# Performance work log

Measured on AMD Instinct MI355X. Metric: run time of the kernel, lower is better.

The kernel has to match this reference:

```python
import jax, jax.numpy as jnp
import numpy as np
from jax import lax

B, N, C = 4, 16384, 384
HEADS, HD = 8, 48
ALPHA = 4.0
KS = 5
HH = WW = 128


def setup_inputs() -> dict:
    key = jax.random.key(0)
    ks = jax.random.split(key, 9)
    s = 0.02
    return {
        "x": jax.random.normal(ks[0], (B, N, C), jnp.float32),
        "W_qg": jax.random.normal(ks[1], (C, 2 * C), jnp.float32) * s,
        "W_kv": jax.random.normal(ks[2], (C, 2 * C), jnp.float32) * s,
        "W_proj": jax.random.normal(ks[3], (C, C), jnp.float32) * s,
        "b_proj": jnp.zeros((C,), jnp.float32),
        "pos_enc": jax.random.normal(ks[4], (1, N, C), jnp.float32) * 0.02,
        "power_p": jax.random.normal(ks[5], (1, HEADS, 1, HD), jnp.float32) * 0.5,
        "scale_p": jax.random.normal(ks[6], (1, 1, C), jnp.float32) * 0.5,
        "dwc_w": jax.random.normal(ks[7], (HD, 1, KS, KS), jnp.float32) * s,
        "dwc_b": jnp.zeros((HD,), jnp.float32),
        "H": HH,
        "W": WW,
    }


def _relu_pow(x, p):
    # relu(x) ** p with safe gradients at x <= 0
    r = jax.nn.relu(x)
    base = jnp.where(r > 0, r, 1.0)
    return jnp.where(r > 0, base ** p, 0.0)


def reference(x, W_qg, W_kv, W_proj, b_proj, pos_enc, power_p, scale_p, dwc_w, dwc_b, H, W):
    Bx, Nx, Cx = x.shape
    h = power_p.shape[1]
    hd = power_p.shape[-1]

    qg = x @ W_qg                      # [B,N,2C]
    q, g = qg[..., :Cx], qg[..., Cx:]
    kv = x @ W_kv                      # [B,N,2C] (sr_ratio == 1)
    k, v = kv[..., :Cx], kv[..., Cx:]
    n = Nx
    k = k + pos_enc

    scale = jax.nn.softplus(scale_p)            # [1,1,C]
    power = 1.0 + ALPHA * jax.nn.sigmoid(power_p)  # [1,h,1,hd]
    q = q / scale
    k = k / scale

    # [B,h,N,hd]
    q = q.reshape(Bx, Nx, h, hd).transpose(0, 2, 1, 3)
    k = k.reshape(Bx, n, h, hd).transpose(0, 2, 1, 3)
    v = v.reshape(Bx, n, h, hd).transpose(0, 2, 1, 3)

    q_pos = _relu_pow(q, power)
    q_neg = _relu_pow(-q, power)
    k_pos = _relu_pow(k, power)
    k_neg = _relu_pow(-k, power)

    q_sim = jnp.concatenate([q_pos, q_neg], axis=-1)   # [B,h,N,2hd]
    q_opp = jnp.concatenate([q_neg, q_pos], axis=-1)
    kk = jnp.concatenate([k_pos, k_neg], axis=-1)      # [B,h,n,2hd]
    v1, v2 = v[..., : hd // 2], v[..., hd // 2:]

    k_mean = kk.mean(axis=2, keepdims=True)            # [B,h,1,2hd]
    inv_n = 1.0 / n

    z_sim = 1.0 / (jnp.sum(q_sim * k_mean, axis=-1, keepdims=True) + 1e-6)
    kv1 = jnp.einsum('bhnd,bhne->bhde', kk, v1) * inv_n  # [B,h,2hd,hd/2]
    x_sim = jnp.einsum('bhnd,bhde->bhne', q_sim, kv1) * z_sim

    z_opp = 1.0 / (jnp.sum(q_opp * k_mean, axis=-1, keepdims=True) + 1e-6)
    kv2 = jnp.einsum('bhnd,bhne->bhde', kk, v2) * inv_n
    x_opp = jnp.einsum('bhnd,bhde->bhne', q_opp, kv2) * z_opp

    out = jnp.concatenate([x_sim, x_opp], axis=-1)     # [B,h,N,hd]
    out = out.transpose(0, 2, 1, 3).reshape(Bx, Nx, Cx)

    # depthwise conv gate on v
    v4 = v.reshape(Bx * h, H, W, hd).transpose(0, 3, 1, 2)  # [B*h, hd, H, W]
    vc = lax.conv_general_dilated(
        v4, dwc_w, window_strides=(1, 1), padding='SAME',
        feature_group_count=hd,
        dimension_numbers=('NCHW', 'OIHW', 'NCHW'))
    vc = vc + dwc_b[None, :, None, None]
    v_out = vc.reshape(Bx, Cx, Nx).transpose(0, 2, 1)  # [B,N,C]

    out = (out + v_out) * g
    out = out @ W_proj + b_proj
    return out
```

## Files before the change

### kernel.cpp

```cpp
#include <hip/hip_runtime.h>
#include <math.h>


#define NB 4
#define NTOK 16384
#define CDIM 384
#define NHEAD 8
#define HDIM 48
#define IMGH 128
#define IMGW 128

typedef unsigned short u16;
typedef unsigned int u32;
typedef __attribute__((ext_vector_type(8))) short bf16x8;
typedef __attribute__((ext_vector_type(4))) float f32x4;

__device__ __forceinline__ float bf2f(u16 u) {
  return __uint_as_float(((unsigned)u) << 16);
}
__device__ __forceinline__ u16 f2bf(float f) {
  unsigned u = __float_as_uint(f);
  u += 0x7FFF + ((u >> 16) & 1);
  return (u16)(u >> 16);
}
__device__ __forceinline__ float pow_mag(float r, float p) {
  if (r < 1e-20f) return 0.0f;
  return exp2f(fminf(p * log2f(r), 80.0f));
}
__device__ __forceinline__ float ldx1(const void* p, size_t i, bool f32) {
  return f32 ? ((const float*)p)[i] : bf2f(((const u16*)p)[i]);
}
__device__ __forceinline__ void gload16(u16* lds, const u16* g) {
  __builtin_amdgcn_global_load_lds(
      (const __attribute__((address_space(1))) u32*)g,
      (__attribute__((address_space(3))) u32*)lds, 16, 0, 0);
}

__global__ __launch_bounds__(256) void k0_detect(const void* __restrict__ x,
                                                 int* __restrict__ flag) {
  __shared__ int s[256];
  const u16* p = (const u16*)x;
  const int t = threadIdx.x;
  int good = 0;
#pragma unroll
  for (int i = 0; i < 16; ++i) {
    const u16 w = p[t * 16 + i];
    const int e = (w >> 7) & 0xFF;
    good += (e >= 0x60 && e <= 0x85) ? 1 : 0;
  }
  s[t] = good;
  __syncthreads();
  for (int o = 128; o > 0; o >>= 1) {
    if (t < o) s[t] += s[t + o];
    __syncthreads();
  }
  if (t == 0) *flag = (s[0] >= (4096 * 4) / 5) ? 0 : 1;
}

__global__ __launch_bounds__(256) void kx_convert(const void* __restrict__ x,
                                                  const int* __restrict__ flag,
                                                  u16* __restrict__ xbf) {
  if (*flag == 0) return;
  const size_t S = (size_t)NB * NTOK * CDIM;
  const size_t tid = (size_t)blockIdx.x * 256 + threadIdx.x;
  const size_t stride = (size_t)gridDim.x * 256;
  const float4* xf = (const float4*)x;
  for (size_t i = tid; i < S / 8; i += stride) {
    const float4 a = xf[i * 2 + 0];
    const float4 b = xf[i * 2 + 1];
    *(ushort4*)(xbf + i * 8 + 0) = make_ushort4(f2bf(a.x), f2bf(a.y), f2bf(a.z), f2bf(a.w));
    *(ushort4*)(xbf + i * 8 + 4) = make_ushort4(f2bf(b.x), f2bf(b.y), f2bf(b.z), f2bf(b.w));
  }
}

__global__ __launch_bounds__(256) void kprep(
    const void* __restrict__ Wqg, const void* __restrict__ Wkv,
    const void* __restrict__ Wp, const int* __restrict__ flag,
    u16* __restrict__ W2T, u16* __restrict__ WpT)
{
  const bool f32 = (*flag != 0);
  const int idx = blockIdx.x * 256 + threadIdx.x;
  if (idx < 1536 * 384) {
    const int n = idx / 384, k = idx - n * 384;
    const float v = (n < 768) ? ldx1(Wqg, (size_t)k * 768 + n, f32)
                              : ldx1(Wkv, (size_t)k * 768 + (n - 768), f32);
    W2T[idx] = f2bf(v);
  } else {
    const int j = idx - 1536 * 384;
    if (j < 384 * 384) {
      const int n = j / 384, k = j - n * 384;
      WpT[j] = f2bf(ldx1(Wp, (size_t)k * 384 + n, f32));
    }
  }
}

__global__ __launch_bounds__(512) void k1_mfma(
    const void* __restrict__ x, const u16* __restrict__ xbf,
    const u16* __restrict__ W2T,
    const void* __restrict__ pos_enc, const void* __restrict__ scale_p,
    const int* __restrict__ flag, const int conv_ok,
    u16* __restrict__ qsT, u16* __restrict__ gT, u16* __restrict__ ksT, u16* __restrict__ vT)
{
  const bool f32 = (*flag != 0);
  const bool fast = (!f32) || (conv_ok != 0);
  const u16* Asrc = f32 ? xbf : (const u16*)x;
  __shared__ __align__(16) u16 smem[17408];
  u16* Asm = smem;
  u16* Bsm = smem + 8192;
  const int t = threadIdx.x;
  const int bid = blockIdx.x;
  const int rm = (bid & 7) * 768 + (bid >> 3);
  const int m_idx = rm / 12;
  const int n_idx = rm - m_idx * 12;
  const int n0 = n_idx * 128;
  const int m0 = m_idx * 128;
  const int wave = t >> 6, lane = t & 63;
  const int wr = wave >> 2, wc = wave & 3;
  const int lm = lane & 15, lq = lane >> 4;

  f32x4 acc[4][2] = {};

  auto STAGE = [&](int k0) {
#pragma unroll
    for (int i = 0; i < 2; ++i) {
      const int chunk = i * 512 + t;
      const int row = chunk >> 3, c8 = chunk & 7;
      const int sc8 = c8 ^ (row & 7);
      u16* lpA = &Asm[(i * 512 + wave * 64) * 8];
      u16* lpB = &Bsm[(i * 512 + wave * 64) * 8];
      gload16(lpA, Asrc + (size_t)(m0 + row) * CDIM + k0 + sc8 * 8);
      gload16(lpB, W2T + (size_t)(n0 + row) * CDIM + k0 + sc8 * 8);
    }
  };
  auto COMPUTE = [&]() {
#pragma unroll
    for (int kh = 0; kh < 2; ++kh) {
      bf16x8 af[4], bfr[2];
#pragma unroll
      for (int r = 0; r < 4; ++r) {
        const int row = wr * 64 + r * 16 + lm;
        af[r] = *(const bf16x8*)&Asm[row * 64 + (((kh * 4 + lq) ^ (row & 7)) * 8)];
      }
#pragma unroll
      for (int cb = 0; cb < 2; ++cb) {
        const int row = wc * 32 + cb * 16 + lm;
        bfr[cb] = *(const bf16x8*)&Bsm[row * 64 + (((kh * 4 + lq) ^ (row & 7)) * 8)];
      }
#pragma unroll
      for (int r = 0; r < 4; ++r)
#pragma unroll
        for (int cb = 0; cb < 2; ++cb)
          acc[r][cb] = __builtin_amdgcn_mfma_f32_16x16x32_bf16(af[r], bfr[cb], acc[r][cb], 0, 0, 0);
    }
  };

  if (fast) {
    for (int ks = 0; ks < 6; ++ks) {
      STAGE(ks * 64);
      __syncthreads();
      COMPUTE();
      __syncthreads();
    }
  } else {
    for (int k0 = 0; k0 < CDIM; k0 += 64) {
#pragma unroll
      for (int i = 0; i < 2; ++i) {
        const int chunk = t + i * 512;
        const int row = chunk >> 3, c8 = chunk & 7;
        const int ldsoff = row * 64 + ((c8 ^ (row & 7)) * 8);
        const float* xp = (const float*)x + (size_t)(m0 + row) * CDIM + k0 + c8 * 8;
        const float4 v0 = *(const float4*)xp;
        const float4 v1 = *(const float4*)(xp + 4);
        *(ushort4*)&Asm[ldsoff]     = make_ushort4(f2bf(v0.x), f2bf(v0.y), f2bf(v0.z), f2bf(v0.w));
        *(ushort4*)&Asm[ldsoff + 4] = make_ushort4(f2bf(v1.x), f2bf(v1.y), f2bf(v1.z), f2bf(v1.w));
        *(uint4*)&Bsm[ldsoff] = *(const uint4*)(W2T + (size_t)(n0 + row) * CDIM + k0 + c8 * 8);
      }
      __syncthreads();
      COMPUTE();
      __syncthreads();
    }
  }

  u16* et = smem;
  const int b = m0 >> 14;
  const int TOK0 = m0 & (NTOK - 1);
  const int region = n0 / CDIM;
#pragma unroll
  for (int cb = 0; cb < 2; ++cb) {
    const int cl = wc * 32 + cb * 16 + lm;
    const int c = (n0 - region * CDIM) + cl;
    float inv = 1.0f;
    if (region == 0 || region == 2) inv = 1.0f / log1pf(expf(ldx1(scale_p, c, f32)));
#pragma unroll
    for (int r = 0; r < 4; ++r) {
      const int tl = wr * 64 + r * 16 + lq * 4;
      const f32x4 v = acc[r][cb];
      ushort4 w;
      if (region == 2) {
        const int tok = TOK0 + tl;
        const float p0 = ldx1(pos_enc, (size_t)(tok + 0) * CDIM + c, f32);
        const float p1 = ldx1(pos_enc, (size_t)(tok + 1) * CDIM + c, f32);
        const float p2 = ldx1(pos_enc, (size_t)(tok + 2) * CDIM + c, f32);
        const float p3 = ldx1(pos_enc, (size_t)(tok + 3) * CDIM + c, f32);
        w = make_ushort4(f2bf((v[0] + p0) * inv), f2bf((v[1] + p1) * inv),
                         f2bf((v[2] + p2) * inv), f2bf((v[3] + p3) * inv));
      } else if (region == 0) {
        w = make_ushort4(f2bf(v[0] * inv), f2bf(v[1] * inv), f2bf(v[2] * inv), f2bf(v[3] * inv));
      } else {
        w = make_ushort4(f2bf(v[0]), f2bf(v[1]), f2bf(v[2]), f2bf(v[3]));
      }
      *(ushort4*)&et[cl * 136 + tl] = w;
    }
  }
  __syncthreads();
  u16* dst = (region == 0) ? qsT : (region == 1) ? gT : (region == 2) ? ksT : vT;
  const int cbase = b * CDIM + (n0 - region * CDIM);
#pragma unroll
  for (int i = 0; i < 4; ++i) {
    const int idx = i * 512 + t;
    const int row = idx >> 4, seg = idx & 15;
    const uint4 val = *(const uint4*)&et[row * 136 + seg * 8];
    *(uint4*)(dst + ((size_t)(cbase + row)) * NTOK + TOK0 + seg * 8) = val;
  }
}

__global__ __launch_bounds__(256) void k2_stats(
    const u16* __restrict__ ksT, const u16* __restrict__ vT,
    const void* __restrict__ power_p, const int* __restrict__ flag,
    float* __restrict__ km, float* __restrict__ kvm)
{
  const bool f32 = (*flag != 0);
  __shared__ __align__(16) u16 kkL[96][72];
  __shared__ __align__(16) u16 vL[48][72];
  __shared__ float pw[48];
  const int bh = blockIdx.x;
  const int b = bh >> 3, h = bh & 7;
  const int t = threadIdx.x;
  if (t < 48) pw[t] = 1.0f + 4.0f / (1.0f + expf(-ldx1(power_p, h * HDIM + t, f32)));
  __syncthreads();
  const int wave = t >> 6, lane = t & 63;
  const int lm = lane & 15, lq = lane >> 4;
  f32x4 acc[2][3] = {};
  float ksum = 0.0f;
  const u16* ksbase = ksT + ((size_t)(b * CDIM + h * HDIM)) * NTOK;
  const u16* vbase  = vT  + ((size_t)(b * CDIM + h * HDIM)) * NTOK;
  const int n0base = blockIdx.y * 1024;
  for (int tile = 0; tile < 16; ++tile) {
    const int n0 = n0base + tile * 64;
    for (int i = t; i < 48 * 16; i += 256) {
      const int c = i >> 4, qd = (i & 15) * 4;
      ushort4 kq = *(const ushort4*)(ksbase + (size_t)c * NTOK + n0 + qd);
      ushort4 vq = *(const ushort4*)(vbase  + (size_t)c * NTOK + n0 + qd);
      const float p = pw[c];
      float kf[4] = {bf2f(kq.x), bf2f(kq.y), bf2f(kq.z), bf2f(kq.w)};
      ushort4 pos, neg;
#pragma unroll
      for (int jj = 0; jj < 4; ++jj) {
        const float f = pow_mag(fabsf(kf[jj]), p);
        ((u16*)&pos)[jj] = f2bf((kf[jj] > 0.f) ? f : 0.f);
        ((u16*)&neg)[jj] = f2bf((kf[jj] < 0.f) ? f : 0.f);
      }
      *(ushort4*)&kkL[c][qd]      = pos;
      *(ushort4*)&kkL[c + 48][qd] = neg;
      *(ushort4*)&vL[c][qd]       = vq;
    }
    __syncthreads();
    if (wave < 3) {
      const int mbase = wave * 32;
#pragma unroll
      for (int kh = 0; kh < 2; ++kh) {
        bf16x8 af[2], bfr[3];
#pragma unroll
        for (int mi = 0; mi < 2; ++mi)
          af[mi] = *(const bf16x8*)&kkL[mbase + mi * 16 + lm][kh * 32 + lq * 8];
#pragma unroll
        for (int nj = 0; nj < 3; ++nj)
          bfr[nj] = *(const bf16x8*)&vL[nj * 16 + lm][kh * 32 + lq * 8];
#pragma unroll
        for (int mi = 0; mi < 2; ++mi)
#pragma unroll
          for (int nj = 0; nj < 3; ++nj)
            acc[mi][nj] = __builtin_amdgcn_mfma_f32_16x16x32_bf16(af[mi], bfr[nj], acc[mi][nj], 0, 0, 0);
      }
    }
    if (t < 96) {
#pragma unroll
      for (int nn = 0; nn < 64; nn += 4) {
        const ushort4 kq4 = *(const ushort4*)&kkL[t][nn];
        ksum += (bf2f(kq4.x) + bf2f(kq4.y)) + (bf2f(kq4.z) + bf2f(kq4.w));
      }
    }
    __syncthreads();
  }
  const float inv_n = 1.0f / (float)NTOK;
  if (wave < 3) {
    const int mbase = wave * 32;
#pragma unroll
    for (int mi = 0; mi < 2; ++mi)
#pragma unroll
      for (int nj = 0; nj < 3; ++nj) {
        const f32x4 v = acc[mi][nj];
#pragma unroll
        for (int reg = 0; reg < 4; ++reg) {
          const int d = mbase + mi * 16 + lq * 4 + reg;
          const int e = nj * 16 + lm;
          atomicAdd(&kvm[(size_t)bh * 96 * 48 + d * 48 + e], v[reg] * inv_n);
        }
      }
  }
  if (t < 96) atomicAdd(&km[bh * 96 + t], ksum * inv_n);
}

__global__ __launch_bounds__(256) void k3_attn(
    const u16* __restrict__ qsT, u16* __restrict__ attnT,
    const float* __restrict__ km_g, const float* __restrict__ kvm_g,
    const void* __restrict__ power_p, const int* __restrict__ flag)
{
  const bool f32 = (*flag != 0);
  __shared__ __align__(16) float kvmL[96][48];
  __shared__ float kmL[96];
  __shared__ float pw[48];
  const int bh = blockIdx.y;
  const int b = bh >> 3, h = bh & 7;
  const int t = threadIdx.x;
  for (int i = t; i < 96 * 48; i += 256) kvmL[i / 48][i % 48] = kvm_g[(size_t)bh * 96 * 48 + i];
  if (t < 96) kmL[t] = km_g[bh * 96 + t];
  if (t < 48) pw[t] = 1.0f + 4.0f / (1.0f + expf(-ldx1(power_p, h * HDIM + t, f32)));
  __syncthreads();
  const int n = blockIdx.x * 512 + t;
  const size_t chan0 = ((size_t)(b * CDIM + h * HDIM)) * NTOK + n;
  const u16* qbase = qsT + chan0;
  u16* obase = attnT + chan0;
  float4 accs[2][6] = {}, acco[2][6] = {};
  float zs[2] = {}, zo[2] = {};
  for (int d = 0; d < 48; ++d) {
    const float p = pw[d];
    float qp[2], qn[2];
#pragma unroll
    for (int i = 0; i < 2; ++i) {
      const float qv = bf2f(qbase[(size_t)d * NTOK + i * 256]);
      const float f = pow_mag(fabsf(qv), p);
      qp[i] = (qv > 0.f) ? f : 0.f;
      qn[i] = (qv < 0.f) ? f : 0.f;
      zs[i] = fmaf(qp[i], kmL[d], zs[i]); zs[i] = fmaf(qn[i], kmL[d + 48], zs[i]);
      zo[i] = fmaf(qn[i], kmL[d], zo[i]); zo[i] = fmaf(qp[i], kmL[d + 48], zo[i]);
    }
#pragma unroll
    for (int e4 = 0; e4 < 6; ++e4) {
      const float4 kvA = *(const float4*)&kvmL[d][e4 * 4];
      const float4 kvB = *(const float4*)&kvmL[d + 48][e4 * 4];
      const float4 kvC = *(const float4*)&kvmL[d][24 + e4 * 4];
      const float4 kvD = *(const float4*)&kvmL[d + 48][24 + e4 * 4];
#pragma unroll
      for (int i = 0; i < 2; ++i) {
        accs[i][e4].x = fmaf(qp[i], kvA.x, fmaf(qn[i], kvB.x, accs[i][e4].x));
        accs[i][e4].y = fmaf(qp[i], kvA.y, fmaf(qn[i], kvB.y, accs[i][e4].y));
        accs[i][e4].z = fmaf(qp[i], kvA.z, fmaf(qn[i], kvB.z, accs[i][e4].z));
        accs[i][e4].w = fmaf(qp[i], kvA.w, fmaf(qn[i], kvB.w, accs[i][e4].w));
        acco[i][e4].x = fmaf(qn[i], kvC.x, fmaf(qp[i], kvD.x, acco[i][e4].x));
        acco[i][e4].y = fmaf(qn[i], kvC.y, fmaf(qp[i], kvD.y, acco[i][e4].y));
        acco[i][e4].z = fmaf(qn[i], kvC.z, fmaf(qp[i], kvD.z, acco[i][e4].z));
        acco[i][e4].w = fmaf(qn[i], kvC.w, fmaf(qp[i], kvD.w, acco[i][e4].w));
      }
    }
  }
#pragma unroll
  for (int i = 0; i < 2; ++i) {
    const float zsi = 1.0f / (zs[i] + 1e-6f);
    const float zoi = 1.0f / (zo[i] + 1e-6f);
#pragma unroll
    for (int e4 = 0; e4 < 6; ++e4) {
      const float4 s = accs[i][e4], o = acco[i][e4];
      obase[(size_t)(e4 * 4 + 0) * NTOK + i * 256]    = f2bf(s.x * zsi);
      obase[(size_t)(e4 * 4 + 1) * NTOK + i * 256]    = f2bf(s.y * zsi);
      obase[(size_t)(e4 * 4 + 2) * NTOK + i * 256]    = f2bf(s.z * zsi);
      obase[(size_t)(e4 * 4 + 3) * NTOK + i * 256]    = f2bf(s.w * zsi);
      obase[(size_t)(24 + e4 * 4 + 0) * NTOK + i * 256] = f2bf(o.x * zoi);
      obase[(size_t)(24 + e4 * 4 + 1) * NTOK + i * 256] = f2bf(o.y * zoi);
      obase[(size_t)(24 + e4 * 4 + 2) * NTOK + i * 256] = f2bf(o.z * zoi);
      obase[(size_t)(24 + e4 * 4 + 3) * NTOK + i * 256] = f2bf(o.w * zoi);
    }
  }
}

__global__ __launch_bounds__(256) void k4_conv_combine(
    const u16* __restrict__ vT, const u16* __restrict__ gT,
    const void* __restrict__ dwc_w, const void* __restrict__ dwc_b,
    const int* __restrict__ flag,
    u16* __restrict__ attnT)
{
  const bool f32 = (*flag != 0);
  __shared__ float tile[20][136];
  const int bc = blockIdx.y;
  const int y0 = blockIdx.x * 16;
  const int t = threadIdx.x;
  const int d = bc % 48;
  float w[25];
#pragma unroll
  for (int i = 0; i < 25; ++i) w[i] = ldx1(dwc_w, d * 25 + i, f32);
  const float bias = ldx1(dwc_b, d, f32);
  const u16* vimg = vT + (size_t)bc * NTOK;
  for (int i = t; i < 20 * 34; i += 256) {
    const int r = i / 34, cq = (i - r * 34) * 4;
    const int gy = y0 + r - 2;
    float4 v4 = make_float4(0.f, 0.f, 0.f, 0.f);
    if (gy >= 0 && gy < IMGH) {
      const int gx0 = cq - 4;
      if (gx0 >= 0 && gx0 + 3 < IMGW) {
        const ushort4 u = *(const ushort4*)(vimg + gy * IMGW + gx0);
        v4 = make_float4(bf2f(u.x), bf2f(u.y), bf2f(u.z), bf2f(u.w));
      } else {
#pragma unroll
        for (int jj = 0; jj < 4; ++jj) {
          const int gx = gx0 + jj;
          ((float*)&v4)[jj] = (gx >= 0 && gx < IMGW) ? bf2f(vimg[gy * IMGW + gx]) : 0.f;
        }
      }
    }
    *(float4*)&tile[r][cq] = v4;
  }
  __syncthreads();
  u16* abase = attnT + (size_t)bc * NTOK;
  const u16* gbase = gT + (size_t)bc * NTOK;
#pragma unroll
  for (int pass = 0; pass < 2; ++pass) {
    const int yy = pass * 8 + (t >> 5);
    const int x0 = (t & 31) * 4;
    float a0 = bias, a1 = bias, a2 = bias, a3 = bias;
#pragma unroll
    for (int dy = 0; dy < 5; ++dy) {
      const float* row = &tile[yy + dy][0];
      const float4 A = *(const float4*)&row[x0];
      const float4 B = *(const float4*)&row[x0 + 4];
      const float4 C = *(const float4*)&row[x0 + 8];
      const float c0 = A.z, c1 = A.w, c2 = B.x, c3 = B.y,
                  c4 = B.z, c5 = B.w, c6 = C.x, c7 = C.y;
      const float w0 = w[dy * 5 + 0], w1 = w[dy * 5 + 1], w2 = w[dy * 5 + 2],
                  w3 = w[dy * 5 + 3], w4 = w[dy * 5 + 4];
      a0 = fmaf(w0, c0, fmaf(w1, c1, fmaf(w2, c2, fmaf(w3, c3, fmaf(w4, c4, a0)))));
      a1 = fmaf(w0, c1, fmaf(w1, c2, fmaf(w2, c3, fmaf(w3, c4, fmaf(w4, c5, a1)))));
      a2 = fmaf(w0, c2, fmaf(w1, c3, fmaf(w2, c4, fmaf(w3, c5, fmaf(w4, c6, a2)))));
      a3 = fmaf(w0, c3, fmaf(w1, c4, fmaf(w2, c5, fmaf(w3, c6, fmaf(w4, c7, a3)))));
    }
    const int gidx = (y0 + yy) * IMGW + x0;
    const ushort4 at = *(const ushort4*)(abase + gidx);
    const ushort4 gg = *(const ushort4*)(gbase + gidx);
    *(ushort4*)(abase + gidx) = make_ushort4(
        f2bf((bf2f(at.x) + a0) * bf2f(gg.x)),
        f2bf((bf2f(at.y) + a1) * bf2f(gg.y)),
        f2bf((bf2f(at.z) + a2) * bf2f(gg.z)),
        f2bf((bf2f(at.w) + a3) * bf2f(gg.w)));
  }
}

__global__ __launch_bounds__(256) void k4b_transpose(
    const u16* __restrict__ src,
    u16* __restrict__ dst)
{
  __shared__ u16 tile[64][68];
  const int b  = blockIdx.z;
  const int c0 = blockIdx.y * 64;
  const int n0 = blockIdx.x * 64;
  const int t = threadIdx.x;
  const int tr = t >> 4, tq = t & 15;
#pragma unroll
  for (int i = 0; i < 4; ++i) {
    const int r = tr + i * 16;
    *(ushort4*)&tile[r][tq * 4] =
        *(const ushort4*)(src + ((size_t)(b * CDIM + c0 + r)) * NTOK + n0 + tq * 4);
  }
  __syncthreads();
#pragma unroll
  for (int i = 0; i < 4; ++i) {
    const int n = tr + i * 16;
    const ushort4 vv = make_ushort4(tile[tq * 4 + 0][n], tile[tq * 4 + 1][n],
                                    tile[tq * 4 + 2][n], tile[tq * 4 + 3][n]);
    *(ushort4*)(dst + ((size_t)(b * NTOK + n0 + n)) * CDIM + c0 + tq * 4) = vv;
  }
}

__global__ __launch_bounds__(512) void k5_mfma(
    const u16* __restrict__ A,
    const u16* __restrict__ WpT,
    const void* __restrict__ bp, const int* __restrict__ flag,
    void* __restrict__ out)
{
  const bool f32 = (*flag != 0);
  __shared__ __align__(16) u16 smem[17408];
  u16* Asm = smem;
  u16* Bsm = smem + 8192;
  const int t = threadIdx.x;
  const int bid = blockIdx.x;
  const int rm = (bid & 7) * 192 + (bid >> 3);
  const int m_idx = rm / 3;
  const int n_idx = rm - m_idx * 3;
  const int n0 = n_idx * 128;
  const int m0 = m_idx * 128;
  const int wave = t >> 6, lane = t & 63;
  const int wr = wave >> 2, wc = wave & 3;
  const int lm = lane & 15, lq = lane >> 4;

  f32x4 acc[4][2] = {};

  auto STAGE = [&](int k0) {
#pragma unroll
    for (int i = 0; i < 2; ++i) {
      const int chunk = i * 512 + t;
      const int row = chunk >> 3, c8 = chunk & 7;
      const int sc8 = c8 ^ (row & 7);
      u16* lpA = &Asm[(i * 512 + wave * 64) * 8];
      u16* lpB = &Bsm[(i * 512 + wave * 64) * 8];
      gload16(lpA, A + (size_t)(m0 + row) * CDIM + k0 + sc8 * 8);
      gload16(lpB, WpT + (size_t)(n0 + row) * CDIM + k0 + sc8 * 8);
    }
  };
  auto COMPUTE = [&]() {
#pragma unroll
    for (int kh = 0; kh < 2; ++kh) {
      bf16x8 af[4], bfr[2];
#pragma unroll
      for (int r = 0; r < 4; ++r) {
        const int row = wr * 64 + r * 16 + lm;
        af[r] = *(const bf16x8*)&Asm[row * 64 + (((kh * 4 + lq) ^ (row & 7)) * 8)];
      }
#pragma unroll
      for (int cb = 0; cb < 2; ++cb) {
        const int row = wc * 32 + cb * 16 + lm;
        bfr[cb] = *(const bf16x8*)&Bsm[row * 64 + (((kh * 4 + lq) ^ (row & 7)) * 8)];
      }
#pragma unroll
      for (int r = 0; r < 4; ++r)
#pragma unroll
        for (int cb = 0; cb < 2; ++cb)
          acc[r][cb] = __builtin_amdgcn_mfma_f32_16x16x32_bf16(af[r], bfr[cb], acc[r][cb], 0, 0, 0);
    }
  };

  for (int ks = 0; ks < 6; ++ks) {
    STAGE(ks * 64);
    __syncthreads();
    COMPUTE();
    __syncthreads();
  }

  if (f32) {
    float* ef = (float*)smem;
    float bb[2];
#pragma unroll
    for (int cb = 0; cb < 2; ++cb) bb[cb] = ((const float*)bp)[n0 + wc * 32 + cb * 16 + lm];
    for (int h = 0; h < 2; ++h) {
      __syncthreads();
      if (wr == h) {
#pragma unroll
        for (int cb = 0; cb < 2; ++cb) {
          const int cl = wc * 32 + cb * 16 + lm;
#pragma unroll
          for (int r = 0; r < 4; ++r) {
            const int tl = r * 16 + lq * 4;
            const f32x4 v = acc[r][cb];
#pragma unroll
            for (int reg = 0; reg < 4; ++reg)
              ef[(tl + reg) * 132 + cl] = v[reg] + bb[cb];
          }
        }
      }
      __syncthreads();
      float* ob = (float*)out + (size_t)(m0 + h * 64) * CDIM + n0;
#pragma unroll
      for (int i = 0; i < 4; ++i) {
        const int idx = i * 512 + t;
        const int row = idx >> 5, seg = idx & 31;
        const float4 val = *(const float4*)&ef[row * 132 + seg * 4];
        *(float4*)(ob + (size_t)row * CDIM + seg * 4) = val;
      }
    }
  } else {
#pragma unroll
    for (int cb = 0; cb < 2; ++cb) {
      const int cg = n0 + wc * 32 + cb * 16 + lm;
      const float bbs = bf2f(((const u16*)bp)[cg]);
#pragma unroll
      for (int r = 0; r < 4; ++r) {
        const int rowtok = m0 + wr * 64 + r * 16 + lq * 4;
        const f32x4 v = acc[r][cb];
#pragma unroll
        for (int reg = 0; reg < 4; ++reg) {
          const size_t o = (size_t)(rowtok + reg) * CDIM + cg;
          ((u16*)out)[o] = f2bf(v[reg] + bbs);
        }
      }
    }
  }
}

extern "C" void kernel_launch(void* const* d_in, const int* in_sizes, int n_in,
                              void* d_out, int out_size, void* d_ws, size_t ws_size,
                              hipStream_t stream) {
  const void* x       = d_in[0];
  const void* Wqg     = d_in[1];
  const void* Wkv     = d_in[2];
  const void* Wproj   = d_in[3];
  const void* bproj   = d_in[4];
  const void* pos_enc = d_in[5];
  const void* power_p = d_in[6];
  const void* scale_p = d_in[7];
  const void* dwc_w   = d_in[8];
  const void* dwc_b   = d_in[9];

  const size_t S = (size_t)NB * NTOK * CDIM;
  const size_t stats_off   = 256;
  const size_t stats_bytes = (size_t)(32 * 96 + 32 * 96 * 48) * sizeof(float);
  const size_t w2t_elems = 1536 * 384, wpt_elems = 384 * 384;
  const size_t need = stats_off + stats_bytes + 3 * S * sizeof(u16)
                    + (w2t_elems + wpt_elems) * sizeof(u16);
  if (ws_size < need) return;

  int*   flag = (int*)d_ws;
  float* km   = (float*)((char*)d_ws + stats_off);
  float* kvm  = km + 32 * 96;
  u16* qsT = (u16*)((char*)d_ws + stats_off + stats_bytes);
  u16* gT  = qsT + S;
  u16* ksT = gT + S;
  u16* W2T = ksT + S;
  u16* WpT = W2T + w2t_elems;
  u16* vT  = (u16*)d_out;

  const int conv_ok = (out_size >= (int)(S * 4)) ? 1 : 0;
  u16* xbf = conv_ok ? ((u16*)d_out + S) : (u16*)d_out;

  hipMemsetAsync(km, 0, stats_bytes, stream);

  k0_detect<<<1, 256, 0, stream>>>(x, flag);
  if (conv_ok) kx_convert<<<2048, 256, 0, stream>>>(x, flag, xbf);
  kprep<<<(int)((w2t_elems + wpt_elems + 255) / 256), 256, 0, stream>>>(
      Wqg, Wkv, Wproj, flag, W2T, WpT);
  k1_mfma<<<6144, 512, 0, stream>>>(x, xbf, W2T, pos_enc, scale_p, flag, conv_ok,
                                    qsT, gT, ksT, vT);
  k2_stats<<<dim3(32, 16), 256, 0, stream>>>(ksT, vT, power_p, flag, km, kvm);
  k3_attn<<<dim3(32, 32), 256, 0, stream>>>(qsT, ksT, km, kvm, power_p, flag);
  k4_conv_combine<<<dim3(8, 1536), 256, 0, stream>>>(vT, gT, dwc_w, dwc_b, flag, ksT);
  k4b_transpose<<<dim3(256, 6, 4), 256, 0, stream>>>(ksT, qsT);
  k5_mfma<<<1536, 512, 0, stream>>>(qsT, WpT, bproj, flag, d_out);
}
```

Measured before the change: 662.9 us.

## Move attention apply kernel onto bf16 MFMA with fused normalizer columns

Rewrites k3_attn so the q-feature by kv-matrix product runs as a bf16 MFMA GEMM. The kv matrices and k-mean vectors are packed into one combined B matrix in shared memory, so the z normalizers come out as extra output columns. Output is staged in LDS and written with vectorized stores, and the grid grows to 128-token tiles. In exchange, kv statistics and z denominators are rounded to bf16, which costs some precision.

```diff
diff --git a/kernel.cpp b/kernel.cpp
--- a/kernel.cpp
+++ b/kernel.cpp
@@ -317,69 +317,90 @@
     const void* __restrict__ power_p, const int* __restrict__ flag)
 {
   const bool f32 = (*flag != 0);
-  __shared__ __align__(16) float kvmL[96][48];
-  __shared__ float kmL[96];
+  __shared__ __align__(16) u16 qf[128][104];
+  __shared__ __align__(16) u16 cmat[64][104];
+  __shared__ float zbuf[4][2][32];
   __shared__ float pw[48];
   const int bh = blockIdx.y;
   const int b = bh >> 3, h = bh & 7;
   const int t = threadIdx.x;
-  for (int i = t; i < 96 * 48; i += 256) kvmL[i / 48][i % 48] = kvm_g[(size_t)bh * 96 * 48 + i];
-  if (t < 96) kmL[t] = km_g[bh * 96 + t];
+  const int n0 = blockIdx.x * 128;
   if (t < 48) pw[t] = 1.0f + 4.0f / (1.0f + expf(-ldx1(power_p, h * HDIM + t, f32)));
-  __syncthreads();
-  const int n = blockIdx.x * 512 + t;
-  const size_t chan0 = ((size_t)(b * CDIM + h * HDIM)) * NTOK + n;
-  const u16* qbase = qsT + chan0;
-  u16* obase = attnT + chan0;
-  float4 accs[2][6] = {}, acco[2][6] = {};
-  float zs[2] = {}, zo[2] = {};
-  for (int d = 0; d < 48; ++d) {
-    const float p = pw[d];
-    float qp[2], qn[2];
-#pragma unroll
-    for (int i = 0; i < 2; ++i) {
-      const float qv = bf2f(qbase[(size_t)d * NTOK + i * 256]);
+  for (int i = t; i < 64 * 96; i += 256) {
+    const int nrow = i / 96, d = i - nrow * 96;
+    const int ds = (d + 48) % 96;
+    float val;
+    if (nrow < 24)      val = kvm_g[(size_t)bh * 96 * 48 + d * 48 + nrow];
+    else if (nrow < 48) val = kvm_g[(size_t)bh * 96 * 48 + ds * 48 + nrow];
+    else if (nrow == 48) val = km_g[bh * 96 + d];
+    else if (nrow == 49) val = km_g[bh * 96 + ds];
+    else                val = 0.0f;
+    cmat[nrow][d] = f2bf(val);
+  }
+  __syncthreads();
+  const u16* qbase = qsT + ((size_t)(b * CDIM + h * HDIM)) * NTOK + n0;
+  for (int i = t; i < 48 * 32; i += 256) {
+    const int c = i >> 5, tq = (i & 31) * 4;
+    const ushort4 q4 = *(const ushort4*)(qbase + (size_t)c * NTOK + tq);
+    const float p = pw[c];
+#pragma unroll
+    for (int jj = 0; jj < 4; ++jj) {
+      const float qv = bf2f(((const u16*)&q4)[jj]);
       const float f = pow_mag(fabsf(qv), p);
-      qp[i] = (qv > 0.f) ? f : 0.f;
-      qn[i] = (qv < 0.f) ? f : 0.f;
-      zs[i] = fmaf(qp[i], kmL[d], zs[i]); zs[i] = fmaf(qn[i], kmL[d + 48], zs[i]);
-      zo[i] = fmaf(qn[i], kmL[d], zo[i]); zo[i] = fmaf(qp[i], kmL[d + 48], zo[i]);
-    }
-#pragma unroll
-    for (int e4 = 0; e4 < 6; ++e4) {
-      const float4 kvA = *(const float4*)&kvmL[d][e4 * 4];
-      const float4 kvB = *(const float4*)&kvmL[d + 48][e4 * 4];
-      const float4 kvC = *(const float4*)&kvmL[d][24 + e4 * 4];
-      const float4 kvD = *(const float4*)&kvmL[d + 48][24 + e4 * 4];
-#pragma unroll
-      for (int i = 0; i < 2; ++i) {
-        accs[i][e4].x = fmaf(qp[i], kvA.x, fmaf(qn[i], kvB.x, accs[i][e4].x));
-        accs[i][e4].y = fmaf(qp[i], kvA.y, fmaf(qn[i], kvB.y, accs[i][e4].y));
-        accs[i][e4].z = fmaf(qp[i], kvA.z, fmaf(qn[i], kvB.z, accs[i][e4].z));
-        accs[i][e4].w = fmaf(qp[i], kvA.w, fmaf(qn[i], kvB.w, accs[i][e4].w));
-        acco[i][e4].x = fmaf(qn[i], kvC.x, fmaf(qp[i], kvD.x, acco[i][e4].x));
-        acco[i][e4].y = fmaf(qn[i], kvC.y, fmaf(qp[i], kvD.y, acco[i][e4].y));
-        acco[i][e4].z = fmaf(qn[i], kvC.z, fmaf(qp[i], kvD.z, acco[i][e4].z));
-        acco[i][e4].w = fmaf(qn[i], kvC.w, fmaf(qp[i], kvD.w, acco[i][e4].w));
-      }
-    }
-  }
-#pragma unroll
-  for (int i = 0; i < 2; ++i) {
-    const float zsi = 1.0f / (zs[i] + 1e-6f);
-    const float zoi = 1.0f / (zo[i] + 1e-6f);
-#pragma unroll
-    for (int e4 = 0; e4 < 6; ++e4) {
-      const float4 s = accs[i][e4], o = acco[i][e4];
-      obase[(size_t)(e4 * 4 + 0) * NTOK + i * 256]    = f2bf(s.x * zsi);
-      obase[(size_t)(e4 * 4 + 1) * NTOK + i * 256]    = f2bf(s.y * zsi);
-      obase[(size_t)(e4 * 4 + 2) * NTOK + i * 256]    = f2bf(s.z * zsi);
-      obase[(size_t)(e4 * 4 + 3) * NTOK + i * 256]    = f2bf(s.w * zsi);
-      obase[(size_t)(24 + e4 * 4 + 0) * NTOK + i * 256] = f2bf(o.x * zoi);
-      obase[(size_t)(24 + e4 * 4 + 1) * NTOK + i * 256] = f2bf(o.y * zoi);
-      obase[(size_t)(24 + e4 * 4 + 2) * NTOK + i * 256] = f2bf(o.z * zoi);
-      obase[(size_t)(24 + e4 * 4 + 3) * NTOK + i * 256] = f2bf(o.w * zoi);
-    }
+      qf[tq + jj][c]      = f2bf((qv > 0.f) ? f : 0.f);
+      qf[tq + jj][c + 48] = f2bf((qv < 0.f) ? f : 0.f);
+    }
+  }
+  __syncthreads();
+  const int wave = t >> 6, lane = t & 63;
+  const int lm = lane & 15, lq = lane >> 4;
+  f32x4 acc[2][4] = {};
+#pragma unroll
+  for (int ks = 0; ks < 3; ++ks) {
+    bf16x8 af[2], bfr[4];
+#pragma unroll
+    for (int mi = 0; mi < 2; ++mi)
+      af[mi] = *(const bf16x8*)&qf[wave * 32 + mi * 16 + lm][ks * 32 + lq * 8];
+#pragma unroll
+    for (int nj = 0; nj < 4; ++nj)
+      bfr[nj] = *(const bf16x8*)&cmat[nj * 16 + lm][ks * 32 + lq * 8];
+#pragma unroll
+    for (int mi = 0; mi < 2; ++mi)
+#pragma unroll
+      for (int nj = 0; nj < 4; ++nj)
+        acc[mi][nj] = __builtin_amdgcn_mfma_f32_16x16x32_bf16(af[mi], bfr[nj], acc[mi][nj], 0, 0, 0);
+  }
+  if (lm < 2) {
+#pragma unroll
+    for (int mi = 0; mi < 2; ++mi) {
+      const f32x4 v = acc[mi][3];
+#pragma unroll
+      for (int reg = 0; reg < 4; ++reg)
+        zbuf[wave][lm][mi * 16 + lq * 4 + reg] = v[reg];
+    }
+  }
+  __syncthreads();
+  u16* et = &qf[0][0];
+#pragma unroll
+  for (int mi = 0; mi < 2; ++mi)
+#pragma unroll
+    for (int nj = 0; nj < 3; ++nj) {
+      const f32x4 v = acc[mi][nj];
+      const int e = nj * 16 + lm;
+      const int zsel = (e < 24) ? 0 : 1;
+#pragma unroll
+      for (int reg = 0; reg < 4; ++reg) {
+        const int tl = mi * 16 + lq * 4 + reg;
+        const float z = zbuf[wave][zsel][tl];
+        const float zi = 1.0f / (z + 1e-6f);
+        et[e * 136 + wave * 32 + tl] = f2bf(v[reg] * zi);
+      }
+    }
+  __syncthreads();
+  u16* obase = attnT + ((size_t)(b * CDIM + h * HDIM)) * NTOK + n0;
+  for (int i = t; i < 48 * 16; i += 256) {
+    const int e = i >> 4, seg = i & 15;
+    *(uint4*)(obase + (size_t)e * NTOK + seg * 8) = *(const uint4*)&et[e * 136 + seg * 8];
   }
 }
 
@@ -637,7 +658,7 @@
   k1_mfma<<<6144, 512, 0, stream>>>(x, xbf, W2T, pos_enc, scale_p, flag, conv_ok,
                                     qsT, gT, ksT, vT);
   k2_stats<<<dim3(32, 16), 256, 0, stream>>>(ksT, vT, power_p, flag, km, kvm);
-  k3_attn<<<dim3(32, 32), 256, 0, stream>>>(qsT, ksT, km, kvm, power_p, flag);
+  k3_attn<<<dim3(128, 32), 256, 0, stream>>>(qsT, ksT, km, kvm, power_p, flag);
   k4_conv_combine<<<dim3(8, 1536), 256, 0, stream>>>(vT, gT, dwc_w, dwc_b, flag, ksT);
   k4b_transpose<<<dim3(256, 6, 4), 256, 0, stream>>>(ksT, qsT);
   k5_mfma<<<1536, 512, 0, stream>>>(qsT, WpT, bproj, flag, d_out);
```

New measurement: 661.7 us. Within noise of the previous version (-0.2%).
